# Kernel optimization log

Measured on AMD Instinct MI355X. Metric: run time of the kernel, lower is better.

## Reference

```python
import jax, jax.numpy as jnp
import numpy as np

T, H, I, SI, E, K = 1024, 2048, 1408, 5632, 8, 4
NORM_TOPK_PROB = False


def setup_inputs() -> dict:
    key = jax.random.key(0)
    ks = jax.random.split(key, 9)
    s = lambda k, shape, fan: (jax.random.normal(k, shape, jnp.float32) * (fan ** -0.5))
    return {
        "hidden_states": jax.random.normal(ks[0], (T, H), jnp.float32),
        "Wg": s(ks[1], (E, H, I), H),   # per-expert gate_proj
        "Wu": s(ks[2], (E, H, I), H),   # per-expert up_proj
        "Wd": s(ks[3], (E, I, H), I),   # per-expert down_proj
        "Wsg": s(ks[4], (H, SI), H),    # shared expert gate_proj
        "Wsu": s(ks[5], (H, SI), H),    # shared expert up_proj
        "Wsd": s(ks[6], (SI, H), SI),   # shared expert down_proj
        "W_router": s(ks[7], (H, E), H),        # self.gate
        "W_shared_gate": s(ks[8], (H, 1), H),   # self.shared_expert_gate
    }


def reference(hidden_states, Wg, Wu, Wd, Wsg, Wsu, Wsd, W_router, W_shared_gate):
    x = hidden_states  # [T, H]
    # shared expert: silu(x Wg) * (x Wu) then down proj (fused_gate_up + matmul)
    shared = (jax.nn.silu(x @ Wsg) * (x @ Wsu)) @ Wsd          # [T, H]
    shared_gate = jax.nn.sigmoid(x @ W_shared_gate)            # [T, 1]
    # router: softmax in float32, then top-k
    probs = jax.nn.softmax((x @ W_router).astype(jnp.float32), axis=-1)  # [T, E]
    top_v, top_i = jax.lax.top_k(probs, K)                     # [T, K]
    if NORM_TOPK_PROB and K > 1:
        top_v = top_v / jnp.sum(top_v, axis=-1, keepdims=True)
    # combine weights: zero for non-routed (expert, token) pairs -> same math
    # as the original gather/expert/scatter(index_add_) loop
    combine = jnp.zeros((T, E), top_v.dtype).at[jnp.arange(T)[:, None], top_i].set(top_v)
    # expert GEMMs (dequantized-GPTQ math): silu(x Wg_e) * (x Wu_e) @ Wd_e
    g = jnp.einsum('th,ehi->eti', x, Wg)                       # [E, T, I]
    u = jnp.einsum('th,ehi->eti', x, Wu)                       # [E, T, I]
    y = jnp.einsum('eti,eih->eth', jax.nn.silu(g) * u, Wd)     # [E, T, H]
    moe = jnp.einsum('eth,te->th', y, combine.astype(x.dtype)) # [T, H]
    scale = 1.0 / (K ** 0.5)
    return (moe + shared_gate * shared) * jnp.asarray(scale, x.dtype)
```

## Files before the change

### kernel.cpp

```cpp
#include <hip/hip_runtime.h>
#include <cstdint>
#include <cstddef>


typedef unsigned short u16;
typedef _Float16 f16;
typedef __attribute__((ext_vector_type(8))) _Float16 half8;
typedef __attribute__((ext_vector_type(4))) float f32x4;

#define GLDS(g, l) __builtin_amdgcn_global_load_lds(                          \
    (const __attribute__((address_space(1))) void*)(g),                       \
    (__attribute__((address_space(3))) void*)(l), 16, 0, 0)

__device__ __forceinline__ float b2f(u16 u){ return __uint_as_float(((uint32_t)u)<<16); }
__device__ __forceinline__ u16 f2b(float f){
  uint32_t x = __float_as_uint(f);
  return (u16)((x + 0x7fffu + ((x>>16)&1u)) >> 16);
}

__global__ __launch_bounds__(64) void detect_kernel(const uint32_t* __restrict__ X,
                                                    int* __restrict__ flag){
  const int lane = threadIdx.x;
  int cnt = 0;
  for (int i = lane; i < 256; i += 64){
    const uint32_t e = (X[i] >> 23) & 0xffu;
    cnt += (e >= 90u && e <= 160u) ? 1 : 0;
  }
#pragma unroll
  for (int off = 32; off > 0; off >>= 1) cnt += __shfl_xor(cnt, off, 64);
  if (lane == 0) *flag = (cnt > 128) ? 1 : 0;
}

template<bool F32>
__device__ void router_conv_body(const void* X, const void* Wr, const void* Wxg,
                                 f16* __restrict__ Xh, float* __restrict__ combine,
                                 float* __restrict__ sgate, float (*red)[9]){
  const int t = blockIdx.x, tid = threadIdx.x, lane = tid&63, wave = tid>>6;
  const int h0 = tid*8;
  float xv[8], gv[8];
  if (F32){
    const float* xp = (const float*)X + (size_t)t*2048 + h0;
    const float4 a = *(const float4*)xp, b = *(const float4*)(xp+4);
    xv[0]=a.x; xv[1]=a.y; xv[2]=a.z; xv[3]=a.w;
    xv[4]=b.x; xv[5]=b.y; xv[6]=b.z; xv[7]=b.w;
    const float* gp = (const float*)Wxg + h0;
    const float4 c = *(const float4*)gp, d = *(const float4*)(gp+4);
    gv[0]=c.x; gv[1]=c.y; gv[2]=c.z; gv[3]=c.w;
    gv[4]=d.x; gv[5]=d.y; gv[6]=d.z; gv[7]=d.w;
  } else {
    union { uint4 v; u16 s[8]; } xr, gr;
    xr.v = *(const uint4*)((const u16*)X + (size_t)t*2048 + h0);
    gr.v = *(const uint4*)((const u16*)Wxg + h0);
#pragma unroll
    for (int q = 0; q < 8; ++q){ xv[q] = b2f(xr.s[q]); gv[q] = b2f(gr.s[q]); }
  }
  half8 h8;
#pragma unroll
  for (int j = 0; j < 8; ++j) h8[j] = (f16)xv[j];
  *(half8*)(Xh + (size_t)t*2048 + h0) = h8;

  float acc[8] = {0,0,0,0,0,0,0,0};
  float ag = 0.f;
#pragma unroll
  for (int jj = 0; jj < 8; ++jj){
    const int h = h0 + jj;
    float w[8];
    if (F32){
      const float* wp = (const float*)Wr + (size_t)h*8;
      const float4 w0 = *(const float4*)wp, w1 = *(const float4*)(wp+4);
      w[0]=w0.x; w[1]=w0.y; w[2]=w0.z; w[3]=w0.w;
      w[4]=w1.x; w[5]=w1.y; w[6]=w1.z; w[7]=w1.w;
    } else {
      union { uint4 v; u16 s[8]; } wv;
      wv.v = *(const uint4*)((const u16*)Wr + (size_t)h*8);
#pragma unroll
      for (int q = 0; q < 8; ++q) w[q] = b2f(wv.s[q]);
    }
#pragma unroll
    for (int e = 0; e < 8; ++e) acc[e] += xv[jj] * w[e];
    ag += xv[jj] * gv[jj];
  }
#pragma unroll
  for (int off = 32; off > 0; off >>= 1){
#pragma unroll
    for (int e = 0; e < 8; ++e) acc[e] += __shfl_xor(acc[e], off, 64);
    ag += __shfl_xor(ag, off, 64);
  }
  if (lane == 0){
#pragma unroll
    for (int e = 0; e < 8; ++e) red[wave][e] = acc[e];
    red[wave][8] = ag;
  }
  __syncthreads();
  if (tid == 0){
    float a[8], g = 0.f;
#pragma unroll
    for (int e = 0; e < 8; ++e) a[e] = red[0][e] + red[1][e] + red[2][e] + red[3][e];
    g = red[0][8] + red[1][8] + red[2][8] + red[3][8];
    float m = a[0];
#pragma unroll
    for (int e = 1; e < 8; ++e) m = fmaxf(m, a[e]);
    float p[8]; float s = 0.f;
#pragma unroll
    for (int e = 0; e < 8; ++e){ p[e] = __expf(a[e]-m); s += p[e]; }
    const float inv = 1.f/s;
#pragma unroll
    for (int e = 0; e < 8; ++e) p[e] *= inv;
#pragma unroll
    for (int e = 0; e < 8; ++e){
      int cnt = 0;
#pragma unroll
      for (int j = 0; j < 8; ++j)
        cnt += (p[j] > p[e]) || (p[j] == p[e] && j < e);
      combine[(size_t)t*8 + e] = (cnt < 4) ? p[e] : 0.f;
    }
    sgate[t] = 1.f/(1.f + __expf(-g));
  }
}
__global__ __launch_bounds__(256) void router_conv(const void* X, const void* Wr, const void* Wxg,
                                                   f16* Xh, float* combine, float* sgate,
                                                   const int* flag){
  __shared__ float red[4][9];
  if (*flag) router_conv_body<true >(X, Wr, Wxg, Xh, combine, sgate, red);
  else       router_conv_body<false>(X, Wr, Wxg, Xh, combine, sgate, red);
}

__global__ __launch_bounds__(1024) void compact_kernel(
    const float* __restrict__ combine, int* __restrict__ cnt,
    int* __restrict__ tok, float* __restrict__ cw, int* __restrict__ inv){
  __shared__ int woff[8][16];
  __shared__ int ccnt[8];
  const int t = threadIdx.x, lane = t&63, wv = t>>6;
  float v[8];
#pragma unroll
  for (int e = 0; e < 8; ++e){
    v[e] = combine[(size_t)t*8 + e];
    const unsigned long long b = __ballot(v[e] > 0.f);
    if (lane == 0) woff[e][wv] = (int)__popcll(b);
  }
  __syncthreads();
  if (t < 8){
    int s = 0;
#pragma unroll
    for (int w = 0; w < 16; ++w){ const int c = woff[t][w]; woff[t][w] = s; s += c; }
    ccnt[t] = s; cnt[t] = s;
  }
  __syncthreads();
  int k = 0;
  const unsigned long long below = (lane == 0) ? 0ull : (~0ull >> (64 - lane));
#pragma unroll
  for (int e = 0; e < 8; ++e){
    const unsigned long long b = __ballot(v[e] > 0.f);
    if (v[e] > 0.f){
      const int p = woff[e][wv] + (int)__popcll(b & below);
      tok[e*1024 + p] = t;
      cw [e*1024 + p] = v[e];
      if (k < 4) inv[t*4 + k] = e*1024 + p;
      ++k;
    }
  }
  for (; k < 4; ++k) inv[t*4 + k] = -1;
#pragma unroll
  for (int e = 0; e < 8; ++e){
    if (t >= ccnt[e]){ tok[e*1024 + t] = 0; cw[e*1024 + t] = 0.f; }
  }
}

#define KP 132
template<bool F32>
__device__ void tcvt_body(const void* S, f16* __restrict__ Dm, int K, int N,
                          size_t soff, int n0, int k0, float* Tf){
  const int t = threadIdx.x;
  const int rg = t >> 4, nc = (t & 15)*4;
#pragma unroll
  for (int sp = 0; sp < 2; ++sp){
    float va[4][4];
#pragma unroll
    for (int r = 0; r < 4; ++r){
      const int kk = sp*64 + rg*4 + r;
      if (F32){
        const float4 vv = *(const float4*)((const float*)S + soff + (size_t)(k0+kk)*N + n0 + nc);
        va[r][0]=vv.x; va[r][1]=vv.y; va[r][2]=vv.z; va[r][3]=vv.w;
      } else {
        union { uint2 u; u16 s[4]; } rr;
        rr.u = *(const uint2*)((const u16*)S + soff + (size_t)(k0+kk)*N + n0 + nc);
#pragma unroll
        for (int j = 0; j < 4; ++j) va[r][j] = b2f(rr.s[j]);
      }
    }
#pragma unroll
    for (int j = 0; j < 4; ++j){
      f32x4 w; w[0]=va[0][j]; w[1]=va[1][j]; w[2]=va[2][j]; w[3]=va[3][j];
      *(f32x4*)(Tf + (size_t)(nc+j)*KP + sp*64 + rg*4) = w;
    }
  }
  __syncthreads();
  const int nr = t >> 4, kq = (t & 15)*8;
#pragma unroll
  for (int q = 0; q < 4; ++q){
    const int n = q*16 + nr;
    const f32x4 a = *(const f32x4*)(Tf + (size_t)n*KP + kq);
    const f32x4 b = *(const f32x4*)(Tf + (size_t)n*KP + kq + 4);
    half8 h;
    h[0]=(f16)a[0]; h[1]=(f16)a[1]; h[2]=(f16)a[2]; h[3]=(f16)a[3];
    h[4]=(f16)b[0]; h[5]=(f16)b[1]; h[6]=(f16)b[2]; h[7]=(f16)b[3];
    *(half8*)(Dm + (size_t)(n0+n)*K + k0 + kq) = h;
  }
}
__global__ __launch_bounds__(256) void tcvt_all(
    const void* Wsg, const void* Wsu, const void* Wg, const void* Wu,
    const void* Wd, const void* Wsd,
    f16* WsgT, f16* WsuT, f16* WgT, f16* WuT, f16* WdT, f16* WsdT,
    const int* flag){
  __shared__ float Tf[64*KP];
  int bid = blockIdx.x;
  const void* S; f16* D; int K, N, nx; size_t soff = 0;
  if (bid < 1408){ S = Wsg; D = WsgT; K = 2048; N = 5632; nx = 88; }
  else if (bid < 2816){ bid -= 1408; S = Wsu; D = WsuT; K = 2048; N = 5632; nx = 88; }
  else if (bid < 5632){
    bid -= 2816; const int z = bid/352; bid -= z*352;
    soff = (size_t)z*2048*1408;
    S = Wg; D = WgT + soff; K = 2048; N = 1408; nx = 22;
  } else if (bid < 8448){
    bid -= 5632; const int z = bid/352; bid -= z*352;
    soff = (size_t)z*2048*1408;
    S = Wu; D = WuT + soff; K = 2048; N = 1408; nx = 22;
  } else if (bid < 11264){ bid -= 8448; S = Wd; D = WdT; K = 11264; N = 2048; nx = 32; }
  else { bid -= 11264; S = Wsd; D = WsdT; K = 5632; N = 2048; nx = 32; }
  const int n0 = (bid % nx)*64, k0 = (bid / nx)*128;
  if (*flag) tcvt_body<true >(S, D, K, N, soff, n0, k0, Tf);
  else       tcvt_body<false>(S, D, K, N, soff, n0, k0, Tf);
}

__device__ __forceinline__ void stage_T128(const f16* __restrict__ Row, int ld, int k0, f16* Ls){
  const int tid = threadIdx.x, wave = tid>>6, lane = tid&63;
#pragma unroll
  for (int i = 0; i < 2; ++i){
    const int rbase = i*64 + wave*16;
    const f16* g = Row + (size_t)(rbase + (lane>>2))*ld + (k0 + (lane&3)*8);
    GLDS(g, Ls + rbase*32);
  }
}
__device__ __forceinline__ void stage_T64(const f16* __restrict__ Row, int ld, int k0, f16* Ls){
  const int tid = threadIdx.x, wave = tid>>6, lane = tid&63;
  const int rbase = wave*16;
  const f16* g = Row + (size_t)(rbase + (lane>>2))*ld + (k0 + (lane&3)*8);
  GLDS(g, Ls + rbase*32);
}

__global__ __launch_bounds__(256) void gu_gemm_t(
    const f16* __restrict__ Xh, const f16* __restrict__ WsgT, const f16* __restrict__ WsuT,
    const f16* __restrict__ WgT, const f16* __restrict__ WuT,
    f16* __restrict__ A1s, f16* __restrict__ P,
    const float* __restrict__ sgate, const float* __restrict__ cw,
    const int* __restrict__ cnt, const int* __restrict__ tok)
{
  __shared__ f16 As[128*32];
  __shared__ f16 Bg[64*32];
  __shared__ f16 Bu[64*32];
  int bid = blockIdx.x;
  const int tid = threadIdx.x, lane = tid&63, wave = tid>>6;
  const f16 *BgRow, *BuRow; f16* outp; const float* rs;
  int ldout, m0, n0;
  const f16 *gA0, *gA1;
  if (bid < 704){
    n0 = (bid % 88)*64; m0 = (bid / 88)*128;
    BgRow = WsgT + (size_t)n0*2048; BuRow = WsuT + (size_t)n0*2048;
    outp = A1s; rs = sgate; ldout = 5632;
    const int r0 = m0 + wave*16 + (lane>>2);
    gA0 = Xh + (size_t)r0*2048 + (lane&3)*8;
    gA1 = gA0 + (size_t)64*2048;
  } else {
    bid -= 704;
    const int e = bid / 176, r = bid % 176;
    const int mt = r / 22;
    if (mt*128 >= cnt[e]) return;
    n0 = (r % 22)*64; m0 = mt*128;
    const size_t off = (size_t)e*1408*2048;
    BgRow = WgT + off + (size_t)n0*2048; BuRow = WuT + off + (size_t)n0*2048;
    outp = P + (size_t)e*1024*1408; rs = cw + e*1024; ldout = 1408;
    const int* tp = tok + e*1024 + m0;
    const int t0 = tp[wave*16 + (lane>>2)];
    const int t1 = tp[64 + wave*16 + (lane>>2)];
    gA0 = Xh + (size_t)t0*2048 + (lane&3)*8;
    gA1 = Xh + (size_t)t1*2048 + (lane&3)*8;
  }
  const int wm = wave>>1, wn = wave&1, lr = lane&15, q = lane>>4;

  const f32x4 z4 = {0.f,0.f,0.f,0.f};
  f32x4 ag[4][2], au[4][2];
#pragma unroll
  for (int mi = 0; mi < 4; ++mi)
#pragma unroll
    for (int ni = 0; ni < 2; ++ni){ ag[mi][ni] = z4; au[mi][ni] = z4; }

  for (int k0 = 0; k0 < 2048; k0 += 32){
    __syncthreads();
    GLDS(gA0 + k0, As + wave*512);
    GLDS(gA1 + k0, As + 2048 + wave*512);
    stage_T64(BgRow, 2048, k0, Bg);
    stage_T64(BuRow, 2048, k0, Bu);
    __syncthreads();
    half8 af[4];
#pragma unroll
    for (int mi = 0; mi < 4; ++mi)
      af[mi] = *(const half8*)(As + (wm*64 + mi*16 + lr)*32 + q*8);
#pragma unroll
    for (int ni = 0; ni < 2; ++ni){
      const half8 bfg = *(const half8*)(Bg + (wn*32 + ni*16 + lr)*32 + q*8);
      const half8 bfu = *(const half8*)(Bu + (wn*32 + ni*16 + lr)*32 + q*8);
#pragma unroll
      for (int mi = 0; mi < 4; ++mi){
        ag[mi][ni] = __builtin_amdgcn_mfma_f32_16x16x32_f16(af[mi], bfg, ag[mi][ni], 0, 0, 0);
        au[mi][ni] = __builtin_amdgcn_mfma_f32_16x16x32_f16(af[mi], bfu, au[mi][ni], 0, 0, 0);
      }
    }
  }

  float rsv[4][4];
#pragma unroll
  for (int mi = 0; mi < 4; ++mi)
#pragma unroll
    for (int r = 0; r < 4; ++r)
      rsv[mi][r] = rs[m0 + wm*64 + mi*16 + q*4 + r];
#pragma unroll
  for (int mi = 0; mi < 4; ++mi)
#pragma unroll
    for (int ni = 0; ni < 2; ++ni)
#pragma unroll
      for (int r = 0; r < 4; ++r){
        const int row = m0 + wm*64 + mi*16 + q*4 + r;
        const int col = n0 + wn*32 + ni*16 + lr;
        const float g = ag[mi][ni][r];
        const float v = (g / (1.f + __expf(-g))) * au[mi][ni][r] * rsv[mi][r];
        outp[(size_t)row*ldout + col] = (f16)v;
      }
}

__global__ __launch_bounds__(256) void down_gemm_t(
    const f16* __restrict__ Pm, const f16* __restrict__ A1s,
    const f16* __restrict__ WdT, const f16* __restrict__ WsdT,
    const int* __restrict__ cnt,
    float* __restrict__ downR, float* __restrict__ shp)
{
  __shared__ f16 As[128*32];
  __shared__ f16 Bs[128*32];
  const int z = blockIdx.z;
  const int m0 = blockIdx.y*128, n0 = blockIdx.x*128;
  const f16 *A, *B; int lda, ldk, KT; float* C;
  if (z < 8){
    if (m0 >= cnt[z]) return;
    A = Pm + (size_t)z*1024*1408 + (size_t)m0*1408; lda = 1408;
    B = WdT + (size_t)z*1408; ldk = 11264; KT = 44;
    C = downR + (size_t)z*1024*2048;
  } else {
    A = A1s + (size_t)(z-8)*2816 + (size_t)m0*5632; lda = 5632;
    B = WsdT + (size_t)(z-8)*2816; ldk = 5632; KT = 88;
    C = shp + (size_t)(z-8)*2097152;
  }
  const f16* Arow = A;
  const f16* Brow = B + (size_t)n0*ldk;
  const int tid = threadIdx.x, lane = tid&63, wave = tid>>6;
  const int wm = wave>>1, wn = wave&1, lr = lane&15, q = lane>>4;

  const f32x4 z4 = {0.f,0.f,0.f,0.f};
  f32x4 acc[4][4];
#pragma unroll
  for (int mi = 0; mi < 4; ++mi)
#pragma unroll
    for (int ni = 0; ni < 4; ++ni) acc[mi][ni] = z4;

  for (int kt = 0; kt < KT; ++kt){
    __syncthreads();
    stage_T128(Arow, lda, kt*32, As);
    stage_T128(Brow, ldk, kt*32, Bs);
    __syncthreads();
    half8 af[4], bf[4];
#pragma unroll
    for (int mi = 0; mi < 4; ++mi)
      af[mi] = *(const half8*)(As + (wm*64 + mi*16 + lr)*32 + q*8);
#pragma unroll
    for (int ni = 0; ni < 4; ++ni)
      bf[ni] = *(const half8*)(Bs + (wn*64 + ni*16 + lr)*32 + q*8);
#pragma unroll
    for (int ni = 0; ni < 4; ++ni)
#pragma unroll
      for (int mi = 0; mi < 4; ++mi)
        acc[mi][ni] = __builtin_amdgcn_mfma_f32_16x16x32_f16(af[mi], bf[ni], acc[mi][ni], 0, 0, 0);
  }
#pragma unroll
  for (int mi = 0; mi < 4; ++mi)
#pragma unroll
    for (int ni = 0; ni < 4; ++ni)
#pragma unroll
      for (int r = 0; r < 4; ++r){
        const int row = m0 + wm*64 + mi*16 + q*4 + r;
        const int col = n0 + wn*64 + ni*16 + lr;
        C[(size_t)row*2048 + col] = acc[mi][ni][r];
      }
}

__global__ __launch_bounds__(256) void final_g(
    const float4* __restrict__ sh0, const float4* __restrict__ sh1,
    const float4* __restrict__ downR, const int* __restrict__ inv,
    void* __restrict__ out, const int* __restrict__ flag){
  const int t = blockIdx.x;
  const int4 iv = *(const int4*)(inv + t*4);
  const int idx[4] = {iv.x, iv.y, iv.z, iv.w};
#pragma unroll
  for (int jj = 0; jj < 2; ++jj){
    const int j = threadIdx.x + jj*256;
    const size_t b = (size_t)t*512 + j;
    const float4 a = sh0[b], c = sh1[b];
    float v0 = a.x + c.x, v1 = a.y + c.y, v2 = a.z + c.z, v3 = a.w + c.w;
#pragma unroll
    for (int k = 0; k < 4; ++k){
      if (idx[k] >= 0){
        const float4 d = downR[(size_t)idx[k]*512 + j];
        v0 += d.x; v1 += d.y; v2 += d.z; v3 += d.w;
      }
    }
    v0 *= 0.5f; v1 *= 0.5f; v2 *= 0.5f; v3 *= 0.5f;
    if (*flag){
      float4 o; o.x=v0; o.y=v1; o.z=v2; o.w=v3;
      ((float4*)out)[b] = o;
    } else {
      uint2 o;
      o.x = (uint32_t)f2b(v0) | ((uint32_t)f2b(v1) << 16);
      o.y = (uint32_t)f2b(v2) | ((uint32_t)f2b(v3) << 16);
      ((uint2*)out)[b] = o;
    }
  }
}

#define LDBT 40
#define ABUF 4096
#define BBUF 2560
struct BR { float v[8]; };
template<bool F32>
__device__ __forceinline__ void loadB(const void* __restrict__ B, size_t ldb, int k0, int n0, BR& r){
  const int t = threadIdx.x, c = t&63, kg = t>>6;
  if (F32){
    const float* p = (const float*)B + (size_t)(k0 + kg*8)*ldb + (n0 + c);
#pragma unroll
    for (int j = 0; j < 8; ++j) r.v[j] = p[(size_t)j*ldb];
  } else {
    const u16* p = (const u16*)B + (size_t)(k0 + kg*8)*ldb + (n0 + c);
#pragma unroll
    for (int j = 0; j < 8; ++j) r.v[j] = b2f(p[(size_t)j*ldb]);
  }
}
__device__ __forceinline__ void storeB(const BR& r, f16* BT){
  const int t = threadIdx.x, c = t&63, kg = t>>6;
  half8 h;
#pragma unroll
  for (int j = 0; j < 8; ++j) h[j] = (f16)r.v[j];
  *(half8*)(BT + c*LDBT + kg*8) = h;
}
template<bool F32>
__device__ void gu_body_r(const f16* __restrict__ Arow, const void* __restrict__ Bgp,
                          const void* __restrict__ Bup, f16* __restrict__ outp,
                          const float* __restrict__ rs, int rs_stride,
                          int ldb, int ldout, int m0, int n0,
                          f16* As, f16* BgT, f16* BuT)
{
  const int tid = threadIdx.x, lane = tid&63, wave = tid>>6;
  const int wm = wave>>1, wn = wave&1, lr = lane&15, q = lane>>4;
  const f32x4 z4 = {0.f,0.f,0.f,0.f};
  f32x4 ag[4][2], au[4][2];
#pragma unroll
  for (int mi = 0; mi < 4; ++mi)
#pragma unroll
    for (int ni = 0; ni < 2; ++ni){ ag[mi][ni] = z4; au[mi][ni] = z4; }
  const int KT = 64;
  BR rg, ru;
  loadB<F32>(Bgp, ldb, 0, n0, rg);
  loadB<F32>(Bup, ldb, 0, n0, ru);
  storeB(rg, BgT); storeB(ru, BuT);
  stage_T128(Arow, 2048, 0, As);
  loadB<F32>(Bgp, ldb, 32, n0, rg);
  loadB<F32>(Bup, ldb, 32, n0, ru);
  __syncthreads();
  for (int kt = 0; kt < KT; ++kt){
    const int cur = kt&1, nxt = cur^1;
    if (kt+1 < KT){
      storeB(rg, BgT + nxt*BBUF);
      storeB(ru, BuT + nxt*BBUF);
      stage_T128(Arow, 2048, (kt+1)*32, As + nxt*ABUF);
    }
    if (kt+2 < KT){
      loadB<F32>(Bgp, ldb, (kt+2)*32, n0, rg);
      loadB<F32>(Bup, ldb, (kt+2)*32, n0, ru);
    }
    const f16* Ac = As + cur*ABUF;
    const f16* Bgc = BgT + cur*BBUF;
    const f16* Buc = BuT + cur*BBUF;
    half8 af[4];
#pragma unroll
    for (int mi = 0; mi < 4; ++mi)
      af[mi] = *(const half8*)(Ac + (wm*64 + mi*16 + lr)*32 + q*8);
#pragma unroll
    for (int ni = 0; ni < 2; ++ni){
      const half8 bfg = *(const half8*)(Bgc + (wn*32 + ni*16 + lr)*LDBT + q*8);
      const half8 bfu = *(const half8*)(Buc + (wn*32 + ni*16 + lr)*LDBT + q*8);
#pragma unroll
      for (int mi = 0; mi < 4; ++mi){
        ag[mi][ni] = __builtin_amdgcn_mfma_f32_16x16x32_f16(af[mi], bfg, ag[mi][ni], 0, 0, 0);
        au[mi][ni] = __builtin_amdgcn_mfma_f32_16x16x32_f16(af[mi], bfu, au[mi][ni], 0, 0, 0);
      }
    }
    __syncthreads();
  }
  float rsv[4][4];
#pragma unroll
  for (int mi = 0; mi < 4; ++mi)
#pragma unroll
    for (int r = 0; r < 4; ++r)
      rsv[mi][r] = rs[(size_t)(m0 + wm*64 + mi*16 + q*4 + r)*rs_stride];
#pragma unroll
  for (int mi = 0; mi < 4; ++mi)
#pragma unroll
    for (int ni = 0; ni < 2; ++ni)
#pragma unroll
      for (int r = 0; r < 4; ++r){
        const int row = m0 + wm*64 + mi*16 + q*4 + r;
        const int col = n0 + wn*32 + ni*16 + lr;
        const float g = ag[mi][ni][r];
        const float v = (g / (1.f + __expf(-g))) * au[mi][ni][r] * rsv[mi][r];
        outp[(size_t)row*ldout + col] = (f16)v;
      }
}
__global__ __launch_bounds__(256) void gu_gemm_r(
    const f16* __restrict__ Xh, const void* Wsg, const void* Wsu,
    const void* Wg, const void* Wu, f16* __restrict__ A1s, f16* __restrict__ P,
    const float* __restrict__ sgate, const float* __restrict__ combine, const int* flag)
{
  __shared__ f16 As[2*ABUF];
  __shared__ f16 BgT[2*BBUF];
  __shared__ f16 BuT[2*BBUF];
  const bool f32v = (*flag != 0);
  int bid = blockIdx.x;
  const void *Bg, *Bu; f16* outp; const float* rs;
  int rs_stride, ldb, ldout, m0, n0;
  if (bid < 704){
    n0 = (bid % 88)*64; m0 = (bid / 88)*128;
    Bg = Wsg; Bu = Wsu; outp = A1s; rs = sgate;
    rs_stride = 1; ldb = 5632; ldout = 5632;
  } else {
    bid -= 704;
    const int e = bid / 176, r = bid % 176;
    n0 = (r % 22)*64; m0 = (r / 22)*128;
    const size_t off = (size_t)e*2048*1408;
    Bg = f32v ? (const void*)((const float*)Wg + off) : (const void*)((const u16*)Wg + off);
    Bu = f32v ? (const void*)((const float*)Wu + off) : (const void*)((const u16*)Wu + off);
    outp = P + (size_t)e*1408; rs = combine + e;
    rs_stride = 8; ldb = 1408; ldout = 11264;
  }
  const f16* Arow = Xh + (size_t)m0*2048;
  if (f32v) gu_body_r<true >(Arow, Bg, Bu, outp, rs, rs_stride, ldb, ldout, m0, n0, As, BgT, BuT);
  else      gu_body_r<false>(Arow, Bg, Bu, outp, rs, rs_stride, ldb, ldout, m0, n0, As, BgT, BuT);
}
template<bool F32>
__device__ void down_body_r(const f16* __restrict__ Arow, int lda, const void* __restrict__ B,
                            float* __restrict__ C, int m0, int n0, f16* As, f16* BT)
{
  const int tid = threadIdx.x, lane = tid&63, wave = tid>>6;
  const int wm = wave>>1, wn = wave&1, lr = lane&15, q = lane>>4;
  const f32x4 z4 = {0.f,0.f,0.f,0.f};
  f32x4 acc[4][2];
#pragma unroll
  for (int mi = 0; mi < 4; ++mi)
#pragma unroll
    for (int ni = 0; ni < 2; ++ni) acc[mi][ni] = z4;
  const int KT = 176;
  BR rb;
  loadB<F32>(B, 2048, 0, n0, rb);
  storeB(rb, BT);
  stage_T128(Arow, lda, 0, As);
  loadB<F32>(B, 2048, 32, n0, rb);
  __syncthreads();
  for (int kt = 0; kt < KT; ++kt){
    const int cur = kt&1, nxt = cur^1;
    if (kt+1 < KT){
      storeB(rb, BT + nxt*BBUF);
      stage_T128(Arow, lda, (kt+1)*32, As + nxt*ABUF);
    }
    if (kt+2 < KT) loadB<F32>(B, 2048, (kt+2)*32, n0, rb);
    const f16* Ac = As + cur*ABUF;
    const f16* Bc = BT + cur*BBUF;
    half8 af[4];
#pragma unroll
    for (int mi = 0; mi < 4; ++mi)
      af[mi] = *(const half8*)(Ac + (wm*64 + mi*16 + lr)*32 + q*8);
#pragma unroll
    for (int ni = 0; ni < 2; ++ni){
      const half8 bf = *(const half8*)(Bc + (wn*32 + ni*16 + lr)*LDBT + q*8);
#pragma unroll
      for (int mi = 0; mi < 4; ++mi)
        acc[mi][ni] = __builtin_amdgcn_mfma_f32_16x16x32_f16(af[mi], bf, acc[mi][ni], 0, 0, 0);
    }
    __syncthreads();
  }
#pragma unroll
  for (int mi = 0; mi < 4; ++mi)
#pragma unroll
    for (int ni = 0; ni < 2; ++ni)
#pragma unroll
      for (int r = 0; r < 4; ++r){
        const int row = m0 + wm*64 + mi*16 + q*4 + r;
        const int col = n0 + wn*32 + ni*16 + lr;
        C[(size_t)row*2048 + col] = acc[mi][ni][r];
      }
}
__global__ __launch_bounds__(256) void down_gemm_r(
    const f16* __restrict__ Pm, const f16* __restrict__ A1s,
    const void* Wd, const void* Wsd,
    float* __restrict__ c0, float* __restrict__ c1, float* __restrict__ c2, const int* flag)
{
  __shared__ f16 As[2*ABUF];
  __shared__ f16 BT[2*BBUF];
  const int z = blockIdx.z;
  const bool f32v = (*flag != 0);
  const f16* A; const void* B; float* C; int lda;
  if (z == 0){ A = Pm; B = Wd; C = c0; lda = 11264; }
  else if (z == 1){
    A = Pm + 5632;
    B = f32v ? (const void*)((const float*)Wd + (size_t)5632*2048)
             : (const void*)((const u16*)Wd + (size_t)5632*2048);
    C = c1; lda = 11264;
  } else { A = A1s; B = Wsd; C = c2; lda = 5632; }
  const int m0 = blockIdx.y*128, n0 = blockIdx.x*64;
  const f16* Arow = A + (size_t)m0*lda;
  if (f32v) down_body_r<true >(Arow, lda, B, C, m0, n0, As, BT);
  else      down_body_r<false>(Arow, lda, B, C, m0, n0, As, BT);
}
__global__ __launch_bounds__(256) void final3(
    const float4* __restrict__ b0, const float4* __restrict__ b1, const float4* __restrict__ b2,
    void* __restrict__ out, const int* flag, int n4){
  const int i = blockIdx.x*256 + threadIdx.x;
  if (i >= n4) return;
  const float4 a = b0[i], b = b1[i], c = b2[i];
  const float v0 = 0.5f*(a.x + b.x + c.x);
  const float v1 = 0.5f*(a.y + b.y + c.y);
  const float v2 = 0.5f*(a.z + b.z + c.z);
  const float v3 = 0.5f*(a.w + b.w + c.w);
  if (*flag){
    float4 o; o.x=v0; o.y=v1; o.z=v2; o.w=v3;
    ((float4*)out)[i] = o;
  } else {
    uint2 o;
    o.x = (uint32_t)f2b(v0) | ((uint32_t)f2b(v1) << 16);
    o.y = (uint32_t)f2b(v2) | ((uint32_t)f2b(v3) << 16);
    ((uint2*)out)[i] = o;
  }
}

extern "C" void kernel_launch(void* const* d_in, const int* in_sizes, int n_in,
                              void* d_out, int out_size, void* d_ws, size_t ws_size,
                              hipStream_t stream)
{
  (void)in_sizes; (void)n_in; (void)out_size;
  const void* x   = d_in[0];
  const void* Wg  = d_in[1];
  const void* Wu  = d_in[2];
  const void* Wd  = d_in[3];
  const void* Wsg = d_in[4];
  const void* Wsu = d_in[5];
  const void* Wsd = d_in[6];
  const void* Wr  = d_in[7];
  const void* Wxg = d_in[8];

  char* ws = (char*)d_ws;
  size_t off = 0;
  auto alloc = [&](size_t bytes)->char*{
    char* p = ws + off; off = (off + bytes + 255) & ~(size_t)255; return p;
  };
  float* combine = (float*)alloc(32768);
  float* sgate   = (float*)alloc(4096);
  int*   flag    = (int*)  alloc(4096);
  int*   cnt     = (int*)  alloc(4096);
  int*   tok     = (int*)  alloc(8*1024*4);
  float* cw      = (float*)alloc(8*1024*4);
  int*   inv     = (int*)  alloc(1024*4*4);
  f16*   Xh      = (f16*)  alloc((size_t)1024*2048*2);
  f16*   A1s     = (f16*)  alloc((size_t)1024*5632*2);
  f16*   P       = (f16*)  alloc((size_t)8*1024*1408*2);
  float* shp     = (float*)alloc((size_t)3*2097152*4);
  float* downR   = (float*)alloc((size_t)8*1024*2048*4);
  f16*   WsgT    = (f16*)  alloc((size_t)5632*2048*2);
  f16*   WsuT    = (f16*)  alloc((size_t)5632*2048*2);
  f16*   WgT     = (f16*)  alloc((size_t)8*1408*2048*2);
  f16*   WuT     = (f16*)  alloc((size_t)8*1408*2048*2);
  f16*   WdT     = (f16*)  alloc((size_t)2048*11264*2);
  f16*   WsdT    = (f16*)  alloc((size_t)2048*5632*2);
  const size_t NEED_FULL = off;

  detect_kernel<<<dim3(1), dim3(64), 0, stream>>>((const uint32_t*)x, flag);
  router_conv<<<dim3(1024), dim3(256), 0, stream>>>(x, Wr, Wxg, Xh, combine, sgate, flag);

  if (ws_size >= NEED_FULL){
    compact_kernel<<<dim3(1), dim3(1024), 0, stream>>>(combine, cnt, tok, cw, inv);
    tcvt_all<<<dim3(12672), dim3(256), 0, stream>>>(
        Wsg, Wsu, Wg, Wu, Wd, Wsd, WsgT, WsuT, WgT, WuT, WdT, WsdT, flag);
    gu_gemm_t<<<dim3(2112), dim3(256), 0, stream>>>(
        Xh, WsgT, WsuT, WgT, WuT, A1s, P, sgate, cw, cnt, tok);
    down_gemm_t<<<dim3(16, 8, 10), dim3(256), 0, stream>>>(P, A1s, WdT, WsdT, cnt, downR, shp);
    final_g<<<dim3(1024), dim3(256), 0, stream>>>(
        (const float4*)shp, (const float4*)(shp + 2097152), (const float4*)downR,
        inv, d_out, flag);
  } else {
    float* b0 = shp;
    float* b1 = shp + 2097152;
    float* b2 = shp + 2*2097152;
    gu_gemm_r<<<dim3(2112), dim3(256), 0, stream>>>(
        Xh, Wsg, Wsu, Wg, Wu, A1s, P, sgate, combine, flag);
    down_gemm_r<<<dim3(32, 8, 3), dim3(256), 0, stream>>>(P, A1s, Wd, Wsd, b0, b1, b2, flag);
    final3<<<dim3(2048), dim3(256), 0, stream>>>(
        (const float4*)b0, (const float4*)b1, (const float4*)b2, d_out, flag, 524288);
  }
}
```

Baseline: 688.8 us.

## Merge router into weight-transpose prep kernel, widen gate/up tiles, remap blocks for XCDs

The router/convert kernel and the weight transpose-convert kernel become one launch (prep_all), which also does the fp32/bf16 format check inline in every block instead of reading a flag. The gate/up GEMM tile grows from 128x64 to 128x128 per block, so each A tile is reused across twice as many columns, at the cost of more accumulator registers and LDS. Both GEMMs now take a flattened block index remapped as (bid&7)*stride + bid>>3, which appears meant to place neighbouring tiles on the same XCD for better L2 reuse. The extra accumulators could reduce occupancy.

```diff
diff --git a/kernel.cpp b/kernel.cpp
--- a/kernel.cpp
+++ b/kernel.cpp
@@ -34,8 +34,8 @@
 template<bool F32>
 __device__ void router_conv_body(const void* X, const void* Wr, const void* Wxg,
                                  f16* __restrict__ Xh, float* __restrict__ combine,
-                                 float* __restrict__ sgate, float (*red)[9]){
-  const int t = blockIdx.x, tid = threadIdx.x, lane = tid&63, wave = tid>>6;
+                                 float* __restrict__ sgate, int t, float (*red)[9]){
+  const int tid = threadIdx.x, lane = tid&63, wave = tid>>6;
   const int h0 = tid*8;
   float xv[8], gv[8];
   if (F32){
@@ -121,8 +121,8 @@
                                                    f16* Xh, float* combine, float* sgate,
                                                    const int* flag){
   __shared__ float red[4][9];
-  if (*flag) router_conv_body<true >(X, Wr, Wxg, Xh, combine, sgate, red);
-  else       router_conv_body<false>(X, Wr, Wxg, Xh, combine, sgate, red);
+  if (*flag) router_conv_body<true >(X, Wr, Wxg, Xh, combine, sgate, blockIdx.x, red);
+  else       router_conv_body<false>(X, Wr, Wxg, Xh, combine, sgate, blockIdx.x, red);
 }
 
 __global__ __launch_bounds__(1024) void compact_kernel(
@@ -207,13 +207,35 @@
     *(half8*)(Dm + (size_t)(n0+n)*K + k0 + kq) = h;
   }
 }
-__global__ __launch_bounds__(256) void tcvt_all(
+
+__global__ __launch_bounds__(256) void prep_all(
+    const void* X, const void* Wr, const void* Wxg,
     const void* Wsg, const void* Wsu, const void* Wg, const void* Wu,
     const void* Wd, const void* Wsd,
-    f16* WsgT, f16* WsuT, f16* WgT, f16* WuT, f16* WdT, f16* WsdT,
-    const int* flag){
+    f16* Xh, float* combine, float* sgate,
+    f16* WsgT, f16* WsuT, f16* WgT, f16* WuT, f16* WdT, f16* WsdT)
+{
   __shared__ float Tf[64*KP];
+  const int tid = threadIdx.x, lane = tid&63, wave = tid>>6;
+  bool f32v;
+  {
+    const uint32_t v = ((const uint32_t*)X)[tid];
+    const uint32_t e = (v >> 23) & 0xffu;
+    const unsigned long long b = __ballot(e >= 90u && e <= 160u);
+    int* sc = (int*)Tf;
+    if (lane == 0) sc[wave] = (int)__popcll(b);
+    __syncthreads();
+    f32v = (sc[0] + sc[1] + sc[2] + sc[3]) > 128;
+    __syncthreads();
+  }
   int bid = blockIdx.x;
+  if (bid < 1024){
+    float (*red)[9] = (float(*)[9])Tf;
+    if (f32v) router_conv_body<true >(X, Wr, Wxg, Xh, combine, sgate, bid, red);
+    else      router_conv_body<false>(X, Wr, Wxg, Xh, combine, sgate, bid, red);
+    return;
+  }
+  bid -= 1024;
   const void* S; f16* D; int K, N, nx; size_t soff = 0;
   if (bid < 1408){ S = Wsg; D = WsgT; K = 2048; N = 5632; nx = 88; }
   else if (bid < 2816){ bid -= 1408; S = Wsu; D = WsuT; K = 2048; N = 5632; nx = 88; }
@@ -228,8 +250,8 @@
   } else if (bid < 11264){ bid -= 8448; S = Wd; D = WdT; K = 11264; N = 2048; nx = 32; }
   else { bid -= 11264; S = Wsd; D = WsdT; K = 5632; N = 2048; nx = 32; }
   const int n0 = (bid % nx)*64, k0 = (bid / nx)*128;
-  if (*flag) tcvt_body<true >(S, D, K, N, soff, n0, k0, Tf);
-  else       tcvt_body<false>(S, D, K, N, soff, n0, k0, Tf);
+  if (f32v) tcvt_body<true >(S, D, K, N, soff, n0, k0, Tf);
+  else      tcvt_body<false>(S, D, K, N, soff, n0, k0, Tf);
 }
 
 __device__ __forceinline__ void stage_T128(const f16* __restrict__ Row, int ld, int k0, f16* Ls){
@@ -256,26 +278,27 @@
     const int* __restrict__ cnt, const int* __restrict__ tok)
 {
   __shared__ f16 As[128*32];
-  __shared__ f16 Bg[64*32];
-  __shared__ f16 Bu[64*32];
-  int bid = blockIdx.x;
+  __shared__ f16 Bg[128*32];
+  __shared__ f16 Bu[128*32];
+  int bid = (int)blockIdx.x;
+  bid = (bid & 7)*132 + (bid >> 3);
   const int tid = threadIdx.x, lane = tid&63, wave = tid>>6;
   const f16 *BgRow, *BuRow; f16* outp; const float* rs;
   int ldout, m0, n0;
   const f16 *gA0, *gA1;
-  if (bid < 704){
-    n0 = (bid % 88)*64; m0 = (bid / 88)*128;
+  if (bid < 352){
+    n0 = (bid % 44)*128; m0 = (bid / 44)*128;
     BgRow = WsgT + (size_t)n0*2048; BuRow = WsuT + (size_t)n0*2048;
     outp = A1s; rs = sgate; ldout = 5632;
     const int r0 = m0 + wave*16 + (lane>>2);
     gA0 = Xh + (size_t)r0*2048 + (lane&3)*8;
     gA1 = gA0 + (size_t)64*2048;
   } else {
-    bid -= 704;
-    const int e = bid / 176, r = bid % 176;
-    const int mt = r / 22;
+    bid -= 352;
+    const int e = bid / 88, r = bid % 88;
+    const int mt = r / 11;
     if (mt*128 >= cnt[e]) return;
-    n0 = (r % 22)*64; m0 = mt*128;
+    n0 = (r % 11)*128; m0 = mt*128;
     const size_t off = (size_t)e*1408*2048;
     BgRow = WgT + off + (size_t)n0*2048; BuRow = WuT + off + (size_t)n0*2048;
     outp = P + (size_t)e*1024*1408; rs = cw + e*1024; ldout = 1408;
@@ -288,27 +311,27 @@
   const int wm = wave>>1, wn = wave&1, lr = lane&15, q = lane>>4;
 
   const f32x4 z4 = {0.f,0.f,0.f,0.f};
-  f32x4 ag[4][2], au[4][2];
-#pragma unroll
-  for (int mi = 0; mi < 4; ++mi)
-#pragma unroll
-    for (int ni = 0; ni < 2; ++ni){ ag[mi][ni] = z4; au[mi][ni] = z4; }
+  f32x4 ag[4][4], au[4][4];
+#pragma unroll
+  for (int mi = 0; mi < 4; ++mi)
+#pragma unroll
+    for (int ni = 0; ni < 4; ++ni){ ag[mi][ni] = z4; au[mi][ni] = z4; }
 
   for (int k0 = 0; k0 < 2048; k0 += 32){
     __syncthreads();
     GLDS(gA0 + k0, As + wave*512);
     GLDS(gA1 + k0, As + 2048 + wave*512);
-    stage_T64(BgRow, 2048, k0, Bg);
-    stage_T64(BuRow, 2048, k0, Bu);
+    stage_T128(BgRow, 2048, k0, Bg);
+    stage_T128(BuRow, 2048, k0, Bu);
     __syncthreads();
     half8 af[4];
 #pragma unroll
     for (int mi = 0; mi < 4; ++mi)
       af[mi] = *(const half8*)(As + (wm*64 + mi*16 + lr)*32 + q*8);
 #pragma unroll
-    for (int ni = 0; ni < 2; ++ni){
-      const half8 bfg = *(const half8*)(Bg + (wn*32 + ni*16 + lr)*32 + q*8);
-      const half8 bfu = *(const half8*)(Bu + (wn*32 + ni*16 + lr)*32 + q*8);
+    for (int ni = 0; ni < 4; ++ni){
+      const half8 bfg = *(const half8*)(Bg + (wn*64 + ni*16 + lr)*32 + q*8);
+      const half8 bfu = *(const half8*)(Bu + (wn*64 + ni*16 + lr)*32 + q*8);
 #pragma unroll
       for (int mi = 0; mi < 4; ++mi){
         ag[mi][ni] = __builtin_amdgcn_mfma_f32_16x16x32_f16(af[mi], bfg, ag[mi][ni], 0, 0, 0);
@@ -326,11 +349,11 @@
 #pragma unroll
   for (int mi = 0; mi < 4; ++mi)
 #pragma unroll
-    for (int ni = 0; ni < 2; ++ni)
+    for (int ni = 0; ni < 4; ++ni)
 #pragma unroll
       for (int r = 0; r < 4; ++r){
         const int row = m0 + wm*64 + mi*16 + q*4 + r;
-        const int col = n0 + wn*32 + ni*16 + lr;
+        const int col = n0 + wn*64 + ni*16 + lr;
         const float g = ag[mi][ni][r];
         const float v = (g / (1.f + __expf(-g))) * au[mi][ni][r] * rsv[mi][r];
         outp[(size_t)row*ldout + col] = (f16)v;
@@ -345,8 +368,11 @@
 {
   __shared__ f16 As[128*32];
   __shared__ f16 Bs[128*32];
-  const int z = blockIdx.z;
-  const int m0 = blockIdx.y*128, n0 = blockIdx.x*128;
+  int gid = (int)blockIdx.x;
+  gid = (gid & 7)*160 + (gid >> 3);
+  const int z = gid >> 7;
+  const int rem = gid & 127;
+  const int m0 = (rem >> 4)*128, n0 = (rem & 15)*128;
   const f16 *A, *B; int lda, ldk, KT; float* C;
   if (z < 8){
     if (m0 >= cnt[z]) return;
@@ -696,19 +722,20 @@
   const size_t NEED_FULL = off;
 
   detect_kernel<<<dim3(1), dim3(64), 0, stream>>>((const uint32_t*)x, flag);
-  router_conv<<<dim3(1024), dim3(256), 0, stream>>>(x, Wr, Wxg, Xh, combine, sgate, flag);
 
   if (ws_size >= NEED_FULL){
+    prep_all<<<dim3(13696), dim3(256), 0, stream>>>(
+        x, Wr, Wxg, Wsg, Wsu, Wg, Wu, Wd, Wsd,
+        Xh, combine, sgate, WsgT, WsuT, WgT, WuT, WdT, WsdT);
     compact_kernel<<<dim3(1), dim3(1024), 0, stream>>>(combine, cnt, tok, cw, inv);
-    tcvt_all<<<dim3(12672), dim3(256), 0, stream>>>(
-        Wsg, Wsu, Wg, Wu, Wd, Wsd, WsgT, WsuT, WgT, WuT, WdT, WsdT, flag);
-    gu_gemm_t<<<dim3(2112), dim3(256), 0, stream>>>(
+    gu_gemm_t<<<dim3(1056), dim3(256), 0, stream>>>(
         Xh, WsgT, WsuT, WgT, WuT, A1s, P, sgate, cw, cnt, tok);
-    down_gemm_t<<<dim3(16, 8, 10), dim3(256), 0, stream>>>(P, A1s, WdT, WsdT, cnt, downR, shp);
+    down_gemm_t<<<dim3(1280), dim3(256), 0, stream>>>(P, A1s, WdT, WsdT, cnt, downR, shp);
     final_g<<<dim3(1024), dim3(256), 0, stream>>>(
         (const float4*)shp, (const float4*)(shp + 2097152), (const float4*)downR,
         inv, d_out, flag);
   } else {
+    router_conv<<<dim3(1024), dim3(256), 0, stream>>>(x, Wr, Wxg, Xh, combine, sgate, flag);
     float* b0 = shp;
     float* b1 = shp + 2097152;
     float* b2 = shp + 2*2097152;
```

New measurement: 937.9 us. 1.36x slower.

## Double-buffer LDS staging in gate-up and down GEMMs to overlap loads with MFMA

Applied to the files above, without the earlier changes.

Both GEMM kernels now use two LDS buffers. The next K-slice is issued with global_load_lds while the current slice is consumed by MFMAs, and partial vmcnt waits plus explicit barriers replace the two __syncthreads per iteration. The goal is to hide global-to-LDS latency behind compute. In exchange, LDS use per block doubles, which may reduce occupancy, and correctness depends on the hand-counted vmcnt(4), which assumes exactly four outstanding loads per stage per thread.

```diff
diff --git a/kernel.cpp b/kernel.cpp
--- a/kernel.cpp
+++ b/kernel.cpp
@@ -255,9 +255,9 @@
     const float* __restrict__ sgate, const float* __restrict__ cw,
     const int* __restrict__ cnt, const int* __restrict__ tok)
 {
-  __shared__ f16 As[128*32];
-  __shared__ f16 Bg[64*32];
-  __shared__ f16 Bu[64*32];
+  __shared__ f16 As[2*4096];
+  __shared__ f16 Bg[2*2048];
+  __shared__ f16 Bu[2*2048];
   int bid = blockIdx.x;
   const int tid = threadIdx.x, lane = tid&63, wave = tid>>6;
   const f16 *BgRow, *BuRow; f16* outp; const float* rs;
@@ -294,27 +294,44 @@
 #pragma unroll
     for (int ni = 0; ni < 2; ++ni){ ag[mi][ni] = z4; au[mi][ni] = z4; }
 
-  for (int k0 = 0; k0 < 2048; k0 += 32){
-    __syncthreads();
-    GLDS(gA0 + k0, As + wave*512);
-    GLDS(gA1 + k0, As + 2048 + wave*512);
-    stage_T64(BgRow, 2048, k0, Bg);
-    stage_T64(BuRow, 2048, k0, Bu);
-    __syncthreads();
+  auto STAGE = [&](int b, int k0){
+    GLDS(gA0 + k0, As + b*4096 + wave*512);
+    GLDS(gA1 + k0, As + b*4096 + 2048 + wave*512);
+    stage_T64(BgRow, 2048, k0, Bg + b*2048);
+    stage_T64(BuRow, 2048, k0, Bu + b*2048);
+  };
+
+  STAGE(0, 0);
+  int cur = 0;
+  for (int kt = 0; kt < 64; ++kt){
+    if (kt < 63){
+      STAGE(cur^1, (kt+1)*32);
+      asm volatile("s_waitcnt vmcnt(4)" ::: "memory");
+    } else {
+      asm volatile("s_waitcnt vmcnt(0)" ::: "memory");
+    }
+    __builtin_amdgcn_s_barrier();
+    __builtin_amdgcn_sched_barrier(0);
+    const f16* Ab  = As + cur*4096;
+    const f16* Bgb = Bg + cur*2048;
+    const f16* Bub = Bu + cur*2048;
     half8 af[4];
 #pragma unroll
     for (int mi = 0; mi < 4; ++mi)
-      af[mi] = *(const half8*)(As + (wm*64 + mi*16 + lr)*32 + q*8);
+      af[mi] = *(const half8*)(Ab + (wm*64 + mi*16 + lr)*32 + q*8);
 #pragma unroll
     for (int ni = 0; ni < 2; ++ni){
-      const half8 bfg = *(const half8*)(Bg + (wn*32 + ni*16 + lr)*32 + q*8);
-      const half8 bfu = *(const half8*)(Bu + (wn*32 + ni*16 + lr)*32 + q*8);
+      const half8 bfg = *(const half8*)(Bgb + (wn*32 + ni*16 + lr)*32 + q*8);
+      const half8 bfu = *(const half8*)(Bub + (wn*32 + ni*16 + lr)*32 + q*8);
 #pragma unroll
       for (int mi = 0; mi < 4; ++mi){
         ag[mi][ni] = __builtin_amdgcn_mfma_f32_16x16x32_f16(af[mi], bfg, ag[mi][ni], 0, 0, 0);
         au[mi][ni] = __builtin_amdgcn_mfma_f32_16x16x32_f16(af[mi], bfu, au[mi][ni], 0, 0, 0);
       }
     }
+    __builtin_amdgcn_sched_barrier(0);
+    __builtin_amdgcn_s_barrier();
+    cur ^= 1;
   }
 
   float rsv[4][4];
@@ -343,8 +360,8 @@
     const int* __restrict__ cnt,
     float* __restrict__ downR, float* __restrict__ shp)
 {
-  __shared__ f16 As[128*32];
-  __shared__ f16 Bs[128*32];
+  __shared__ f16 As[2*4096];
+  __shared__ f16 Bs[2*4096];
   const int z = blockIdx.z;
   const int m0 = blockIdx.y*128, n0 = blockIdx.x*128;
   const f16 *A, *B; int lda, ldk, KT; float* C;
@@ -370,23 +387,39 @@
 #pragma unroll
     for (int ni = 0; ni < 4; ++ni) acc[mi][ni] = z4;
 
+  auto STAGE = [&](int b, int k0){
+    stage_T128(Arow, lda, k0, As + b*4096);
+    stage_T128(Brow, ldk, k0, Bs + b*4096);
+  };
+
+  STAGE(0, 0);
+  int cur = 0;
   for (int kt = 0; kt < KT; ++kt){
-    __syncthreads();
-    stage_T128(Arow, lda, kt*32, As);
-    stage_T128(Brow, ldk, kt*32, Bs);
-    __syncthreads();
+    if (kt + 1 < KT){
+      STAGE(cur^1, (kt+1)*32);
+      asm volatile("s_waitcnt vmcnt(4)" ::: "memory");
+    } else {
+      asm volatile("s_waitcnt vmcnt(0)" ::: "memory");
+    }
+    __builtin_amdgcn_s_barrier();
+    __builtin_amdgcn_sched_barrier(0);
+    const f16* Ab = As + cur*4096;
+    const f16* Bb = Bs + cur*4096;
     half8 af[4], bf[4];
 #pragma unroll
     for (int mi = 0; mi < 4; ++mi)
-      af[mi] = *(const half8*)(As + (wm*64 + mi*16 + lr)*32 + q*8);
+      af[mi] = *(const half8*)(Ab + (wm*64 + mi*16 + lr)*32 + q*8);
 #pragma unroll
     for (int ni = 0; ni < 4; ++ni)
-      bf[ni] = *(const half8*)(Bs + (wn*64 + ni*16 + lr)*32 + q*8);
+      bf[ni] = *(const half8*)(Bb + (wn*64 + ni*16 + lr)*32 + q*8);
 #pragma unroll
     for (int ni = 0; ni < 4; ++ni)
 #pragma unroll
       for (int mi = 0; mi < 4; ++mi)
         acc[mi][ni] = __builtin_amdgcn_mfma_f32_16x16x32_f16(af[mi], bf[ni], acc[mi][ni], 0, 0, 0);
+    __builtin_amdgcn_sched_barrier(0);
+    __builtin_amdgcn_s_barrier();
+    cur ^= 1;
   }
 #pragma unroll
   for (int mi = 0; mi < 4; ++mi)
```

Result: slower. 707.7 us (+2.7%).
